# Kernel optimization log

Measured on AMD Instinct MI355X. Metric: run time of the kernel, lower is better.

## Reference

```python
import jax, jax.numpy as jnp
import numpy as np

C = 64            # x_channel (d_model)
D = 2 * C         # d_inner (expand=2)
N = C // 2        # d_state
K = 4             # scan directions
R = -(-C // 16)   # dt_rank = ceil(d_model/16)
Bsz, H, W = 2, 48, 48
EPS = 1e-5


def setup_inputs() -> dict:
    key = jax.random.key(0)
    ks = jax.random.split(key, 8)
    g = lambda k, shp, s: jax.random.normal(k, shp, dtype=jnp.float32) * s
    return {
        "fufea1": g(ks[0], (Bsz, C, H, W), 1.0),
        "ln_g": jnp.ones((C,), jnp.float32),
        "ln_b": jnp.zeros((C,), jnp.float32),
        "in_proj_w": g(ks[1], (2 * D, C), C ** -0.5),
        "conv_w": g(ks[2], (D, 1, 3, 3), 1.0 / 3.0),   # depthwise 3x3
        "conv_b": g(ks[3], (D,), 0.02),
        "x_proj_w": g(ks[4], (K, R + 2 * N, D), D ** -0.5),
        "dt_w": g(ks[5], (K, D, R), R ** -0.5),
        "dt_b": g(ks[6], (K, D), 0.1),
        "A_logs": jnp.log(jnp.tile(jnp.arange(1, N + 1, dtype=jnp.float32), (K, D, 1))),  # S4D-real init
        "Ds": jnp.ones((K, D), jnp.float32),
        "out_ln_g": jnp.ones((D,), jnp.float32),
        "out_ln_b": jnp.zeros((D,), jnp.float32),
        "out_proj_w": g(ks[7], (C, D), D ** -0.5),
    }


def _layernorm(x, g, b):
    mu = x.mean(-1, keepdims=True)
    var = ((x - mu) ** 2).mean(-1, keepdims=True)
    return (x - mu) * jax.lax.rsqrt(var + EPS) * g + b


def reference(fufea1, ln_g, ln_b, in_proj_w, conv_w, conv_b, x_proj_w,
              dt_w, dt_b, A_logs, Ds, out_ln_g, out_ln_b, out_proj_w):
    B, Cc, Hh, Ww = fufea1.shape
    L = Hh * Ww
    # pre-LN (over channels, channels-last)
    xn = _layernorm(fufea1.transpose(0, 2, 3, 1), ln_g, ln_b)          # (B,H,W,C)
    # SS2D: in_proj -> split x,z
    xz = xn @ in_proj_w.T                                               # (B,H,W,2D)
    x, z = jnp.split(xz, 2, axis=-1)
    x = x.transpose(0, 3, 1, 2)                                         # (B,D,H,W)
    x = jax.lax.conv_general_dilated(x, conv_w, (1, 1), "SAME",
                                     feature_group_count=D,
                                     dimension_numbers=("NCHW", "OIHW", "NCHW"))
    x = jax.nn.silu(x + conv_b[None, :, None, None])
    # 4-direction sequences: row-major, col-major, and their reverses
    x_hw = x.reshape(B, D, L)
    x_wh = x.transpose(0, 1, 3, 2).reshape(B, D, L)
    xs = jnp.stack([x_hw, x_wh], axis=1)                                # (B,2,D,L)
    xs = jnp.concatenate([xs, jnp.flip(xs, axis=-1)], axis=1)           # (B,K,D,L)
    # per-direction projections of dt, B, C
    x_dbl = jnp.einsum("bkdl,kcd->bkcl", xs, x_proj_w)
    dts, Bs, Cs = jnp.split(x_dbl, [R, R + N], axis=2)                  # (B,K,R,L),(B,K,N,L),(B,K,N,L)
    dts = jnp.einsum("bkrl,kdr->bkdl", dts, dt_w)
    delta = jax.nn.softplus(dts + dt_b[None, :, :, None])               # (B,K,D,L)
    A = -jnp.exp(A_logs)                                                # (K,D,N)
    # selective scan over L; carry h: (B,K,D,N)
    u_l = xs.transpose(3, 0, 1, 2)                                      # (L,B,K,D)
    dt_l = delta.transpose(3, 0, 1, 2)
    B_l = Bs.transpose(3, 0, 1, 2)                                      # (L,B,K,N)
    C_l = Cs.transpose(3, 0, 1, 2)

    def step(h, inp):
        u_t, d_t, b_t, c_t = inp
        dA = jnp.exp(d_t[..., None] * A)                                # (B,K,D,N)
        h = dA * h + (d_t * u_t)[..., None] * b_t[:, :, None, :]
        y = jnp.einsum("bkdn,bkn->bkd", h, c_t)
        return h, y

    h0 = jnp.zeros((B, K, D, N), xs.dtype)
    _, ys = jax.lax.scan(step, h0, (u_l, dt_l, B_l, C_l))               # ys: (L,B,K,D)
    out_y = ys.transpose(1, 2, 3, 0) + Ds[None, :, :, None] * xs        # (B,K,D,L)
    # merge the 4 directions back to row-major hw order
    inv_y = jnp.flip(out_y[:, 2:4], axis=-1)                            # (B,2,D,L)
    wh = lambda t: t.reshape(B, D, Ww, Hh).transpose(0, 1, 3, 2).reshape(B, D, L)
    y = out_y[:, 0] + inv_y[:, 0] + wh(out_y[:, 1]) + wh(inv_y[:, 1])   # (B,D,L)
    y = y.transpose(0, 2, 1).reshape(B, Hh, Ww, D)
    y = _layernorm(y, out_ln_g, out_ln_b) * jax.nn.silu(z)
    out = (y @ out_proj_w.T).transpose(0, 3, 1, 2) + fufea1             # residual add
    return out
```

## Files before the change

kernel.cpp:

```cpp
#include <hip/hip_runtime.h>

#define Cc 64
#define Dd 128
#define Nn 32
#define Kk 4
#define Rr 4
#define Bb 2
#define Hh 48
#define Ww 48
#define Ll 2304
#define EPSf 1e-5f
#define LCc 144

#if __has_builtin(__builtin_amdgcn_exp2f)
#define EXP2F __builtin_amdgcn_exp2f
#else
#define EXP2F exp2f
#endif

__device__ __forceinline__ float wsum64(float v) {
  v += __shfl_xor(v, 32);
  v += __shfl_xor(v, 16);
  v += __shfl_xor(v, 8);
  v += __shfl_xor(v, 4);
  v += __shfl_xor(v, 2);
  v += __shfl_xor(v, 1);
  return v;
}

__device__ __forceinline__ float hmax32(float v) {
  v = fmaxf(v, __shfl_xor(v, 1));
  v = fmaxf(v, __shfl_xor(v, 2));
  v = fmaxf(v, __shfl_xor(v, 4));
  v = fmaxf(v, __shfl_xor(v, 8));
  v = fmaxf(v, __shfl_xor(v, 16));
  return v;
}

__global__ __launch_bounds__(256) void k1_ln_inproj(
    const float* __restrict__ x, const float* __restrict__ g,
    const float* __restrict__ bta, const float* __restrict__ Wp,
    float* __restrict__ xin, float* __restrict__ zb)
{
  __shared__ float xS[16][65];
  __shared__ float xnS[16][64];
  __shared__ float xaS[128][17];
  const int tid = threadIdx.x;
  const int wv = tid >> 6, lane = tid & 63;
  const int pbase = blockIdx.x * 16;
  const int b = pbase / Ll;
  const int lbase = pbase % Ll;
  {
    const int c = tid >> 2, li0 = (tid & 3) * 4;
    const float4 v4 = *(const float4*)&x[(b * Cc + c) * Ll + lbase + li0];
    xS[li0 + 0][c] = v4.x;
    xS[li0 + 1][c] = v4.y;
    xS[li0 + 2][c] = v4.z;
    xS[li0 + 3][c] = v4.w;
  }
  __syncthreads();
  const float gv = g[lane], bv = bta[lane];
  for (int pi = 0; pi < 4; ++pi) {
    const int p = wv * 4 + pi;
    const float v = xS[p][lane];
    const float mu = wsum64(v) * (1.0f / 64.0f);
    const float dv = v - mu;
    const float var = wsum64(dv * dv) * (1.0f / 64.0f);
    const float rs = rsqrtf(var + EPSf);
    xnS[p][lane] = dv * rs * gv + bv;
  }
  __syncthreads();
  float acc[4][4];
  #pragma unroll
  for (int pi = 0; pi < 4; ++pi)
    #pragma unroll
    for (int m = 0; m < 4; ++m) acc[pi][m] = 0.f;
  const float4* W4 = (const float4*)Wp;
  #pragma unroll 4
  for (int c4 = 0; c4 < 16; ++c4) {
    float4 xn4[4];
    #pragma unroll
    for (int pi = 0; pi < 4; ++pi)
      xn4[pi] = ((const float4*)xnS[wv * 4 + pi])[c4];
    #pragma unroll
    for (int m = 0; m < 4; ++m) {
      const float4 w4 = W4[(lane + 64 * m) * 16 + c4];
      #pragma unroll
      for (int pi = 0; pi < 4; ++pi)
        acc[pi][m] += xn4[pi].x * w4.x + xn4[pi].y * w4.y +
                      xn4[pi].z * w4.z + xn4[pi].w * w4.w;
    }
  }
  #pragma unroll
  for (int pi = 0; pi < 4; ++pi) {
    const int l = lbase + wv * 4 + pi;
    zb[(b * Ll + l) * Dd + lane]      = acc[pi][2];
    zb[(b * Ll + l) * Dd + lane + 64] = acc[pi][3];
    xaS[lane][wv * 4 + pi]      = acc[pi][0];
    xaS[lane + 64][wv * 4 + pi] = acc[pi][1];
  }
  __syncthreads();
  const int d = tid >> 1, off = (tid & 1) * 8;
  float* dst = &xin[(b * Dd + d) * Ll + lbase + off];
  #pragma unroll
  for (int i = 0; i < 8; ++i) dst[i] = xaS[d][off + i];
}

__global__ __launch_bounds__(512) void k3_proj(
    const float* __restrict__ xin, const float* __restrict__ cw,
    const float* __restrict__ cb, const float* __restrict__ xpw,
    const float* __restrict__ dtw, const float* __restrict__ dtb,
    float* __restrict__ xc, float2* __restrict__ dd2,
    float* __restrict__ Bm, float* __restrict__ Cm)
{
  __shared__ float xinS[128][30];
  __shared__ float xvS[8][132];
  __shared__ float dtsS[8][16];
  const int t = threadIdx.x;
  const int pb = blockIdx.x * 8;
  const int b = pb / Ll;
  const int lb = pb % Ll;
  const int h0 = lb / Ww, w0 = lb % Ww;
  for (int i = t; i < 3840; i += 512) {
    const int d = i / 30, j = i % 30;
    const int r = j / 10, c = j % 10;
    const int hh = h0 + r - 1, ww = w0 + c - 1;
    float v = 0.f;
    if (hh >= 0 && hh < Hh && ww >= 0 && ww < Ww)
      v = xin[(b * Dd + d) * Ll + hh * Ww + ww];
    xinS[d][j] = v;
  }
  __syncthreads();
  for (int i = t; i < 1024; i += 512) {
    const int pi = i >> 7, d = i & 127;
    float acc = cb[d];
    #pragma unroll
    for (int r = 0; r < 3; ++r)
      #pragma unroll
      for (int c = 0; c < 3; ++c)
        acc += xinS[d][r * 10 + pi + c] * cw[d * 9 + r * 3 + c];
    const float sig = 1.0f / (1.0f + __expf(-acc));
    xvS[pi][d] = acc * sig;
  }
  __syncthreads();
  if (t < 272) {
    const int k = t / 68, c = t % 68;
    const size_t bkL = (size_t)(b * Kk + k) * Ll;
    float acc[8];
    #pragma unroll
    for (int pi = 0; pi < 8; ++pi) acc[pi] = 0.f;
    const float4* w4p = (const float4*)(xpw + (k * 68 + c) * 128);
    for (int d4 = 0; d4 < 32; ++d4) {
      const float4 w4 = w4p[d4];
      #pragma unroll
      for (int pi = 0; pi < 8; ++pi) {
        const float4 x4 = ((const float4*)xvS[pi])[d4];
        acc[pi] += x4.x * w4.x + x4.y * w4.y + x4.z * w4.z + x4.w * w4.w;
      }
    }
    #pragma unroll
    for (int pi = 0; pi < 8; ++pi) {
      const int l0 = lb + pi;
      const int h = l0 / Ww, w = l0 % Ww;
      int lk;
      if      (k == 0) lk = l0;
      else if (k == 1) lk = w * Hh + h;
      else if (k == 2) lk = Ll - 1 - l0;
      else             lk = Ll - 1 - (w * Hh + h);
      if (c < Rr)            dtsS[pi][k * 4 + c] = acc[pi];
      else if (c < Rr + Nn)  Bm[(bkL + lk) * Nn + (c - Rr)] = acc[pi];
      else                   Cm[(bkL + lk) * Nn + (c - Rr - Nn)] = acc[pi];
    }
  } else {
    for (int i = t - 272; i < 1024; i += 240) {
      const int d = i >> 3, pi = i & 7;
      xc[(b * Dd + d) * Ll + lb + pi] = xvS[pi][d];
    }
  }
  __syncthreads();
  {
    const int k = t >> 7, dd = t & 127;
    const float4 dw = *(const float4*)&dtw[(k * Dd + dd) * 4];
    const float biasv = dtb[k * Dd + dd];
    float2* drow = dd2 + ((size_t)((b * Kk + k) * Dd) + dd) * Ll;
    float2 buf[8];
    #pragma unroll
    for (int pi = 0; pi < 8; ++pi) {
      const float a = biasv
          + dtsS[pi][k * 4 + 0] * dw.x + dtsS[pi][k * 4 + 1] * dw.y
          + dtsS[pi][k * 4 + 2] * dw.z + dtsS[pi][k * 4 + 3] * dw.w;
      const float sp = (a > 20.f) ? a : log1pf(__expf(a));
      buf[pi] = make_float2(sp, sp * xvS[pi][dd]);
    }
    if (k == 0) {
      float4* f4 = (float4*)(drow + lb);
      #pragma unroll
      for (int j = 0; j < 4; ++j)
        f4[j] = make_float4(buf[2 * j].x, buf[2 * j].y, buf[2 * j + 1].x, buf[2 * j + 1].y);
    } else if (k == 2) {
      float4* f4 = (float4*)(drow + (Ll - 8 - lb));
      #pragma unroll
      for (int j = 0; j < 4; ++j)
        f4[j] = make_float4(buf[7 - 2 * j].x, buf[7 - 2 * j].y, buf[6 - 2 * j].x, buf[6 - 2 * j].y);
    } else {
      #pragma unroll
      for (int pi = 0; pi < 8; ++pi) {
        const int l0 = lb + pi;
        const int h = l0 / Ww, w = l0 % Ww;
        int lk = w * Hh + h;
        if (k == 3) lk = Ll - 1 - lk;
        drow[lk] = buf[pi];
      }
    }
  }
}

__global__ __launch_bounds__(512) void k4_scan(
    const float2* __restrict__ dd2, const float* __restrict__ Bm,
    const float* __restrict__ Cm, const float* __restrict__ Alogs,
    float* __restrict__ ys)
{
  __shared__ float hendS[16][32];
  __shared__ float carryS[16][32];
  __shared__ float sumDS[16];
  __shared__ float cmaxS[16];
  __shared__ float pS[16][8][36];
  const int tid = threadIdx.x;
  const int s = tid >> 5, n = tid & 31;
  const int blk = blockIdx.x;
  const int bk = blk & 7;
  const int d = blk >> 3;
  const int b = bk >> 2, k = bk & 3;
  const float An = -__expf(Alogs[(k * Dd + d) * Nn + n]);
  const float AnE = An * 1.44269504f;
  const size_t bkL = (size_t)(b * Kk + k) * Ll;
  const float2* dP = dd2 + ((size_t)((b * Kk + k) * Dd) + d) * Ll;
  const float* bP = Bm + bkL * Nn + n;
  const float* cP = Cm + bkL * Nn + n;
  const int lbeg = s * LCc;
  float* yP = ys + ((size_t)((b * Kk + k) * Dd) + d) * Ll + lbeg;
  const int rrow = n & 7, qtr = n >> 3;

  float h = 0.f, sumD = 0.f, cmx = 0.f;
  {
    const float4* q4 = (const float4*)(dP + lbeg);
    const float* bl = bP + (size_t)lbeg * Nn;
    const float* cl = cP + (size_t)lbeg * Nn;
    float4 qa[2], qb[2];
    float bv[2][4], cv[2][4];
    #pragma unroll
    for (int i = 0; i < 2; ++i) {
      qa[i] = q4[2 * i]; qb[i] = q4[2 * i + 1];
      #pragma unroll
      for (int j = 0; j < 4; ++j) {
        bv[i][j] = bl[(4 * i + j) * Nn];
        cv[i][j] = cl[(4 * i + j) * Nn];
      }
    }
    q4 += 4; bl += 8 * Nn; cl += 8 * Nn;
    for (int t8 = 0; t8 < LCc / 8; ++t8) {
      #pragma unroll
      for (int half = 0; half < 2; ++half) {
        const float4 a = qa[half], bq = qb[half];
        const float B0 = bv[half][0], B1 = bv[half][1], B2 = bv[half][2], B3 = bv[half][3];
        const float C0 = cv[half][0], C1 = cv[half][1], C2 = cv[half][2], C3 = cv[half][3];
        qa[half] = q4[0]; qb[half] = q4[1];
        bv[half][0] = bl[0]; bv[half][1] = bl[Nn];
        bv[half][2] = bl[2 * Nn]; bv[half][3] = bl[3 * Nn];
        cv[half][0] = cl[0]; cv[half][1] = cl[Nn];
        cv[half][2] = cl[2 * Nn]; cv[half][3] = cl[3 * Nn];
        q4 += 2; bl += 4 * Nn; cl += 4 * Nn;
        h = EXP2F(a.x * AnE) * h + a.y * B0;  pS[s][half * 4 + 0][n] = h * C0;
        h = EXP2F(a.z * AnE) * h + a.w * B1;  pS[s][half * 4 + 1][n] = h * C1;
        h = EXP2F(bq.x * AnE) * h + bq.y * B2; pS[s][half * 4 + 2][n] = h * C2;
        h = EXP2F(bq.z * AnE) * h + bq.w * B3; pS[s][half * 4 + 3][n] = h * C3;
        sumD += (a.x + a.z) + (bq.x + bq.z);
        cmx = fmaxf(cmx, fmaxf(fmaxf(fabsf(C0), fabsf(C1)),
                               fmaxf(fabsf(C2), fabsf(C3))));
      }
      const float4 a4 = *(const float4*)&pS[s][rrow][qtr * 8];
      const float4 d4v = *(const float4*)&pS[s][rrow][qtr * 8 + 4];
      float sum = ((a4.x + a4.y) + (a4.z + a4.w)) + ((d4v.x + d4v.y) + (d4v.z + d4v.w));
      sum += __shfl_xor(sum, 8);
      sum += __shfl_xor(sum, 16);
      if (n < 8) yP[t8 * 8 + n] = sum;
    }
  }
  hendS[s][n] = h;
  const float cmxAll = hmax32(cmx);
  if (n == 0) { sumDS[s] = sumD; cmaxS[s] = cmxAll; }
  __syncthreads();
  if (tid < 32) {
    float carry = 0.f;
    #pragma unroll
    for (int s2 = 0; s2 < 16; ++s2) {
      carryS[s2][tid] = carry;
      carry = EXP2F(AnE * sumDS[s2]) * carry + hendS[s2][tid];
    }
  }
  __syncthreads();
  const float carry = carryS[s][n];
  const float mc = hmax32(fabsf(carry));
  const float AmaxE = hmax32(AnE);
  const float Pstop = log2f(mc * cmaxS[s] * 3.2e6f) / (-AmaxE);
  {
    float hc = carry, P = 0.f;
    const float4* q4 = (const float4*)(dP + lbeg);
    const float* cl = cP + (size_t)lbeg * Nn;
    for (int t8 = 0; t8 < LCc / 8; ++t8) {
      if (!(P < Pstop)) break;
      #pragma unroll
      for (int half = 0; half < 2; ++half) {
        const float4 qa = q4[0], qb = q4[1];
        q4 += 2;
        hc *= EXP2F(qa.x * AnE); pS[s][half * 4 + 0][n] = hc * cl[0];
        hc *= EXP2F(qa.z * AnE); pS[s][half * 4 + 1][n] = hc * cl[Nn];
        hc *= EXP2F(qb.x * AnE); pS[s][half * 4 + 2][n] = hc * cl[2 * Nn];
        hc *= EXP2F(qb.z * AnE); pS[s][half * 4 + 3][n] = hc * cl[3 * Nn];
        P += (qa.x + qa.z) + (qb.x + qb.z);
        cl += 4 * Nn;
      }
      const float4 a4 = *(const float4*)&pS[s][rrow][qtr * 8];
      const float4 d4v = *(const float4*)&pS[s][rrow][qtr * 8 + 4];
      float sum = ((a4.x + a4.y) + (a4.z + a4.w)) + ((d4v.x + d4v.y) + (d4v.z + d4v.w));
      sum += __shfl_xor(sum, 8);
      sum += __shfl_xor(sum, 16);
      if (n < 8) yP[t8 * 8 + n] += sum;
    }
  }
}

__global__ __launch_bounds__(256) void k5_merge(
    const float* __restrict__ ys, const float* __restrict__ zb,
    const float* __restrict__ og, const float* __restrict__ ob,
    const float* __restrict__ Wo, const float* __restrict__ resid,
    const float* __restrict__ xc, const float* __restrict__ DsP,
    float* __restrict__ out)
{
  __shared__ float ysS[4][16][128];
  __shared__ float tS[16][128];
  __shared__ float oS[64][17];
  __shared__ float xcS[16][128];
  const int tid = threadIdx.x;
  const int wv = tid >> 6, lane = tid & 63;
  const int tb = blockIdx.x;
  const int b = tb / 144;
  const int ti = tb % 144;
  const int tr = ti / 12, tc = ti % 12;
  const int h0 = tr * 4, w0 = tc * 4;
  {
    const int dch = tid & 127, half = tid >> 7;
    #pragma unroll
    for (int ii = 0; ii < 2; ++ii) {
      const int i = half * 2 + ii;
      const int l0 = (h0 + i) * Ww + w0;
      float4 v;
      v = *(const float4*)&xc[(b * Dd + dch) * Ll + l0];
      xcS[i * 4 + 0][dch] = v.x; xcS[i * 4 + 1][dch] = v.y;
      xcS[i * 4 + 2][dch] = v.z; xcS[i * 4 + 3][dch] = v.w;
      v = *(const float4*)&ys[((size_t)(b * Kk + 0) * Dd + dch) * Ll + l0];
      ysS[0][i * 4 + 0][dch] = v.x; ysS[0][i * 4 + 1][dch] = v.y;
      ysS[0][i * 4 + 2][dch] = v.z; ysS[0][i * 4 + 3][dch] = v.w;
      const int r2 = Ll - 4 - (h0 + i) * Ww - w0;
      v = *(const float4*)&ys[((size_t)(b * Kk + 2) * Dd + dch) * Ll + r2];
      ysS[2][i * 4 + 3][dch] = v.x; ysS[2][i * 4 + 2][dch] = v.y;
      ysS[2][i * 4 + 1][dch] = v.z; ysS[2][i * 4 + 0][dch] = v.w;
    }
    #pragma unroll
    for (int jj = 0; jj < 2; ++jj) {
      const int j = half * 2 + jj;
      const int l1 = (w0 + j) * Hh + h0;
      float4 v = *(const float4*)&ys[((size_t)(b * Kk + 1) * Dd + dch) * Ll + l1];
      ysS[1][0 * 4 + j][dch] = v.x; ysS[1][1 * 4 + j][dch] = v.y;
      ysS[1][2 * 4 + j][dch] = v.z; ysS[1][3 * 4 + j][dch] = v.w;
      const int r3 = Ll - 4 - (w0 + j) * Hh - h0;
      v = *(const float4*)&ys[((size_t)(b * Kk + 3) * Dd + dch) * Ll + r3];
      ysS[3][3 * 4 + j][dch] = v.x; ysS[3][2 * 4 + j][dch] = v.y;
      ysS[3][1 * 4 + j][dch] = v.z; ysS[3][0 * 4 + j][dch] = v.w;
    }
  }
  float sDs[2];
  #pragma unroll
  for (int m = 0; m < 2; ++m) {
    const int dch = lane + 64 * m;
    sDs[m] = DsP[dch] + DsP[Dd + dch] + DsP[2 * Dd + dch] + DsP[3 * Dd + dch];
  }
  __syncthreads();
  for (int pi = 0; pi < 4; ++pi) {
    const int p = wv * 4 + pi;
    const int l0 = (h0 + (p >> 2)) * Ww + w0 + (p & 3);
    float tv[2];
    #pragma unroll
    for (int m = 0; m < 2; ++m) {
      const int dch = lane + 64 * m;
      tv[m] = ysS[0][p][dch] + ysS[1][p][dch] + ysS[2][p][dch] + ysS[3][p][dch]
            + sDs[m] * xcS[p][dch];
    }
    const float mu = wsum64(tv[0] + tv[1]) * (1.0f / 128.0f);
    const float q = wsum64((tv[0] - mu) * (tv[0] - mu) +
                           (tv[1] - mu) * (tv[1] - mu)) * (1.0f / 128.0f);
    const float rs = rsqrtf(q + EPSf);
    #pragma unroll
    for (int m = 0; m < 2; ++m) {
      const int dch = lane + 64 * m;
      const float zz = zb[(size_t)(b * Ll + l0) * Dd + dch];
      const float sig = 1.0f / (1.0f + __expf(-zz));
      tS[p][dch] = ((tv[m] - mu) * rs * og[dch] + ob[dch]) * (zz * sig);
    }
  }
  __syncthreads();
  float acc[4] = {0.f, 0.f, 0.f, 0.f};
  const float4* W4 = (const float4*)Wo;
  for (int d4 = 0; d4 < 32; ++d4) {
    const float4 w4 = W4[lane * 32 + d4];
    #pragma unroll
    for (int pi = 0; pi < 4; ++pi) {
      const float4 t4 = ((const float4*)tS[wv * 4 + pi])[d4];
      acc[pi] += t4.x * w4.x + t4.y * w4.y + t4.z * w4.z + t4.w * w4.w;
    }
  }
  #pragma unroll
  for (int pi = 0; pi < 4; ++pi) oS[lane][wv * 4 + pi] = acc[pi];
  __syncthreads();
  const int c = tid >> 2, q = tid & 3;
  const size_t obase = (size_t)(b * Cc + c) * Ll + (size_t)(h0 + q) * Ww + w0;
  const float4 r4 = *(const float4*)(resid + obase);
  float4 o4;
  o4.x = oS[c][q * 4 + 0] + r4.x;
  o4.y = oS[c][q * 4 + 1] + r4.y;
  o4.z = oS[c][q * 4 + 2] + r4.z;
  o4.w = oS[c][q * 4 + 3] + r4.w;
  *(float4*)(out + obase) = o4;
}

extern "C" void kernel_launch(void* const* d_in, const int* in_sizes, int n_in,
                              void* d_out, int out_size, void* d_ws, size_t ws_size,
                              hipStream_t stream)
{
  (void)in_sizes; (void)n_in; (void)out_size; (void)ws_size;
  const float* fufea1     = (const float*)d_in[0];
  const float* ln_g       = (const float*)d_in[1];
  const float* ln_b       = (const float*)d_in[2];
  const float* in_proj_w  = (const float*)d_in[3];
  const float* conv_w     = (const float*)d_in[4];
  const float* conv_b     = (const float*)d_in[5];
  const float* x_proj_w   = (const float*)d_in[6];
  const float* dt_w       = (const float*)d_in[7];
  const float* dt_b       = (const float*)d_in[8];
  const float* A_logs     = (const float*)d_in[9];
  const float* Ds         = (const float*)d_in[10];
  const float* out_ln_g   = (const float*)d_in[11];
  const float* out_ln_b   = (const float*)d_in[12];
  const float* out_proj_w = (const float*)d_in[13];

  float* ws = (float*)d_ws;
  float2* dd2 = (float2*)ws;
  float* Bm   = ws + 4718592;
  float* Cm   = ws + 5308416;
  float* zb   = ws + 5898240;
  float* xc   = ws + 6488064;
  float* ysb  = ws + 7077888;
  float* xin  = ws + 7077888;

  k1_ln_inproj<<<288, 256, 0, stream>>>(fufea1, ln_g, ln_b, in_proj_w, xin, zb);
  k3_proj<<<576, 512, 0, stream>>>(xin, conv_w, conv_b, x_proj_w, dt_w, dt_b,
                                   xc, dd2, Bm, Cm);
  k4_scan<<<1024, 512, 0, stream>>>(dd2, Bm, Cm, A_logs, ysb);
  k5_merge<<<288, 256, 0, stream>>>(ysb, zb, out_ln_g, out_ln_b, out_proj_w, fufea1,
                                    xc, Ds, (float*)d_out);
}
```

Before: 208.0 us.

## Store xin and xc channels-last and shorten scan prefetch depth

```diff
diff --git a/kernel.cpp b/kernel.cpp
--- a/kernel.cpp
+++ b/kernel.cpp
@@ -44,7 +44,6 @@
 {
   __shared__ float xS[16][65];
   __shared__ float xnS[16][64];
-  __shared__ float xaS[128][17];
   const int tid = threadIdx.x;
   const int wv = tid >> 6, lane = tid & 63;
   const int pbase = blockIdx.x * 16;
@@ -94,16 +93,12 @@
   #pragma unroll
   for (int pi = 0; pi < 4; ++pi) {
     const int l = lbase + wv * 4 + pi;
-    zb[(b * Ll + l) * Dd + lane]      = acc[pi][2];
-    zb[(b * Ll + l) * Dd + lane + 64] = acc[pi][3];
-    xaS[lane][wv * 4 + pi]      = acc[pi][0];
-    xaS[lane + 64][wv * 4 + pi] = acc[pi][1];
-  }
-  __syncthreads();
-  const int d = tid >> 1, off = (tid & 1) * 8;
-  float* dst = &xin[(b * Dd + d) * Ll + lbase + off];
-  #pragma unroll
-  for (int i = 0; i < 8; ++i) dst[i] = xaS[d][off + i];
+    const size_t base = (size_t)(b * Ll + l) * Dd;
+    xin[base + lane]      = acc[pi][0];
+    xin[base + lane + 64] = acc[pi][1];
+    zb[base + lane]       = acc[pi][2];
+    zb[base + lane + 64]  = acc[pi][3];
+  }
 }
 
 __global__ __launch_bounds__(512) void k3_proj(
@@ -113,7 +108,7 @@
     float* __restrict__ xc, float2* __restrict__ dd2,
     float* __restrict__ Bm, float* __restrict__ Cm)
 {
-  __shared__ float xinS[128][30];
+  __shared__ float xinS[128][31];
   __shared__ float xvS[8][132];
   __shared__ float dtsS[8][16];
   const int t = threadIdx.x;
@@ -122,12 +117,12 @@
   const int lb = pb % Ll;
   const int h0 = lb / Ww, w0 = lb % Ww;
   for (int i = t; i < 3840; i += 512) {
-    const int d = i / 30, j = i % 30;
+    const int d = i & 127, j = i >> 7;
     const int r = j / 10, c = j % 10;
     const int hh = h0 + r - 1, ww = w0 + c - 1;
     float v = 0.f;
     if (hh >= 0 && hh < Hh && ww >= 0 && ww < Ww)
-      v = xin[(b * Dd + d) * Ll + hh * Ww + ww];
+      v = xin[((size_t)(b * Ll) + hh * Ww + ww) * Dd + d];
     xinS[d][j] = v;
   }
   __syncthreads();
@@ -173,8 +168,8 @@
     }
   } else {
     for (int i = t - 272; i < 1024; i += 240) {
-      const int d = i >> 3, pi = i & 7;
-      xc[(b * Dd + d) * Ll + lb + pi] = xvS[pi][d];
+      const int pi = i >> 7, d = i & 127;
+      xc[((size_t)(b * Ll) + lb + pi) * Dd + d] = xvS[pi][d];
     }
   }
   __syncthreads();
@@ -246,37 +241,25 @@
     const float4* q4 = (const float4*)(dP + lbeg);
     const float* bl = bP + (size_t)lbeg * Nn;
     const float* cl = cP + (size_t)lbeg * Nn;
-    float4 qa[2], qb[2];
-    float bv[2][4], cv[2][4];
-    #pragma unroll
-    for (int i = 0; i < 2; ++i) {
-      qa[i] = q4[2 * i]; qb[i] = q4[2 * i + 1];
-      #pragma unroll
-      for (int j = 0; j < 4; ++j) {
-        bv[i][j] = bl[(4 * i + j) * Nn];
-        cv[i][j] = cl[(4 * i + j) * Nn];
-      }
-    }
-    q4 += 4; bl += 8 * Nn; cl += 8 * Nn;
+    float4 qa = q4[0], qb = q4[1];
+    float b0 = bl[0], b1 = bl[Nn], b2 = bl[2 * Nn], b3 = bl[3 * Nn];
+    float c0 = cl[0], c1 = cl[Nn], c2 = cl[2 * Nn], c3 = cl[3 * Nn];
     for (int t8 = 0; t8 < LCc / 8; ++t8) {
       #pragma unroll
       for (int half = 0; half < 2; ++half) {
-        const float4 a = qa[half], bq = qb[half];
-        const float B0 = bv[half][0], B1 = bv[half][1], B2 = bv[half][2], B3 = bv[half][3];
-        const float C0 = cv[half][0], C1 = cv[half][1], C2 = cv[half][2], C3 = cv[half][3];
-        qa[half] = q4[0]; qb[half] = q4[1];
-        bv[half][0] = bl[0]; bv[half][1] = bl[Nn];
-        bv[half][2] = bl[2 * Nn]; bv[half][3] = bl[3 * Nn];
-        cv[half][0] = cl[0]; cv[half][1] = cl[Nn];
-        cv[half][2] = cl[2 * Nn]; cv[half][3] = cl[3 * Nn];
         q4 += 2; bl += 4 * Nn; cl += 4 * Nn;
-        h = EXP2F(a.x * AnE) * h + a.y * B0;  pS[s][half * 4 + 0][n] = h * C0;
-        h = EXP2F(a.z * AnE) * h + a.w * B1;  pS[s][half * 4 + 1][n] = h * C1;
-        h = EXP2F(bq.x * AnE) * h + bq.y * B2; pS[s][half * 4 + 2][n] = h * C2;
-        h = EXP2F(bq.z * AnE) * h + bq.w * B3; pS[s][half * 4 + 3][n] = h * C3;
-        sumD += (a.x + a.z) + (bq.x + bq.z);
-        cmx = fmaxf(cmx, fmaxf(fmaxf(fabsf(C0), fabsf(C1)),
-                               fmaxf(fabsf(C2), fabsf(C3))));
+        const float4 qa_n = q4[0], qb_n = q4[1];
+        const float b0n = bl[0], b1n = bl[Nn], b2n = bl[2 * Nn], b3n = bl[3 * Nn];
+        const float c0n = cl[0], c1n = cl[Nn], c2n = cl[2 * Nn], c3n = cl[3 * Nn];
+        h = EXP2F(qa.x * AnE) * h + qa.y * b0; pS[s][half * 4 + 0][n] = h * c0;
+        h = EXP2F(qa.z * AnE) * h + qa.w * b1; pS[s][half * 4 + 1][n] = h * c1;
+        h = EXP2F(qb.x * AnE) * h + qb.y * b2; pS[s][half * 4 + 2][n] = h * c2;
+        h = EXP2F(qb.z * AnE) * h + qb.w * b3; pS[s][half * 4 + 3][n] = h * c3;
+        sumD += (qa.x + qa.z) + (qb.x + qb.z);
+        cmx = fmaxf(cmx, fmaxf(fmaxf(fabsf(c0), fabsf(c1)),
+                               fmaxf(fabsf(c2), fabsf(c3))));
+        qa = qa_n; qb = qb_n; b0 = b0n; b1 = b1n; b2 = b2n; b3 = b3n;
+        c0 = c0n; c1 = c1n; c2 = c2n; c3 = c3n;
       }
       const float4 a4 = *(const float4*)&pS[s][rrow][qtr * 8];
       const float4 d4v = *(const float4*)&pS[s][rrow][qtr * 8 + 4];
@@ -349,15 +332,19 @@
   const int tr = ti / 12, tc = ti % 12;
   const int h0 = tr * 4, w0 = tc * 4;
   {
+    const int p = tid >> 4, qq = tid & 15;
+    const int l0 = (h0 + (p >> 2)) * Ww + w0 + (p & 3);
+    const float4* src = (const float4*)&xc[((size_t)(b * Ll) + l0) * Dd];
+    ((float4*)xcS[p])[qq]      = src[qq];
+    ((float4*)xcS[p])[qq + 16] = src[qq + 16];
+  }
+  {
     const int dch = tid & 127, half = tid >> 7;
     #pragma unroll
     for (int ii = 0; ii < 2; ++ii) {
       const int i = half * 2 + ii;
       const int l0 = (h0 + i) * Ww + w0;
       float4 v;
-      v = *(const float4*)&xc[(b * Dd + dch) * Ll + l0];
-      xcS[i * 4 + 0][dch] = v.x; xcS[i * 4 + 1][dch] = v.y;
-      xcS[i * 4 + 2][dch] = v.z; xcS[i * 4 + 3][dch] = v.w;
       v = *(const float4*)&ys[((size_t)(b * Kk + 0) * Dd + dch) * Ll + l0];
       ysS[0][i * 4 + 0][dch] = v.x; ysS[0][i * 4 + 1][dch] = v.y;
       ysS[0][i * 4 + 2][dch] = v.z; ysS[0][i * 4 + 3][dch] = v.w;
```

Measured after the change: 201.0 us. 3.3% less time.
